# Kernel tuning notes

Hardware: AMD Instinct MI355X
Metric: run time of the kernel (lower is better)

The kernel has to match this reference:

```python
import jax, jax.numpy as jnp
import numpy as np

EPS = 1e-5  # BatchNorm eps


def _conv(x, w, pad):
    # NCHW / OIHW stride-1 convolution (matches nn.Conv2d(..., padding=pad, bias=False))
    return jax.lax.conv_general_dilated(
        x, w, window_strides=(1, 1), padding=[(pad, pad), (pad, pad)],
        dimension_numbers=("NCHW", "OIHW", "NCHW"))


def _bn2d(x, g, b, m, v):
    # inference-mode BN folded to a per-channel affine
    s = g * jax.lax.rsqrt(v + EPS)
    return x * s[None, :, None, None] + (b - m * s)[None, :, None, None]


def _pool2(x):
    # AvgPool2d(2): non-overlapping 2x2 mean
    n, c, h, w = x.shape
    return x.reshape(n, c, h // 2, 2, w // 2, 2).mean(axis=(3, 5))


def _block(x, w, g, b, m, v):
    # Conv -> BN -> ReLU -> AvgPool2 -> Hardtanh(0,1)
    x = _conv(x, w, pad=2)
    x = _bn2d(x, g, b, m, v)
    x = jax.nn.relu(x)
    x = _pool2(x)
    return jnp.clip(x, 0.0, 1.0)


def setup_inputs() -> dict:
    key = jax.random.key(0)
    ks = jax.random.split(key, 24)
    B = 1024
    x = jax.random.uniform(ks[0], (B, 3, 32, 32), dtype=jnp.float32)

    def wgt(k, shape):
        fan_in = shape[1] * shape[2] * shape[3]
        return jax.random.normal(k, shape, jnp.float32) / np.float32(np.sqrt(fan_in))

    def bn(k, c):
        k1, k2, k3, k4 = jax.random.split(k, 4)
        g = jax.random.uniform(k1, (c,), jnp.float32, 0.5, 1.5)
        b = jax.random.normal(k2, (c,), jnp.float32) * 0.1
        m = jax.random.normal(k3, (c,), jnp.float32) * 0.1
        v = jax.random.uniform(k4, (c,), jnp.float32, 0.5, 1.5)
        return g, b, m, v

    w1 = wgt(ks[1], (32, 3, 5, 5))
    w2 = wgt(ks[2], (32, 32, 5, 5))
    w3 = wgt(ks[3], (64, 32, 5, 5))
    w4 = wgt(ks[4], (10, 64, 4, 4))  # fc1 as a 4x4 valid conv
    g1, b1, m1, v1 = bn(ks[5], 32)
    g2, b2, m2, v2 = bn(ks[6], 32)
    g3, b3, m3, v3 = bn(ks[7], 64)
    g4, b4, m4, v4 = bn(ks[8], 10)
    return dict(x=x,
                w1=w1, g1=g1, b1=b1, m1=m1, v1=v1,
                w2=w2, g2=g2, b2=b2, m2=m2, v2=v2,
                w3=w3, g3=g3, b3=b3, m3=m3, v3=v3,
                w4=w4, g4=g4, b4=b4, m4=m4, v4=v4)


def reference(x,
              w1, g1, b1, m1, v1,
              w2, g2, b2, m2, v2,
              w3, g3, b3, m3, v3,
              w4, g4, b4, m4, v4):
    x = _block(x, w1, g1, b1, m1, v1)   # [B,32,16,16]
    x = _block(x, w2, g2, b2, m2, v2)   # [B,32,8,8]
    x = _block(x, w3, g3, b3, m3, v3)   # [B,64,4,4]
    x = _conv(x, w4, pad=0)             # [B,10,1,1]
    x = x.reshape(x.shape[0], -1)       # flatten -> [B,10]
    s = g4 * jax.lax.rsqrt(v4 + EPS)    # BatchNorm1d_fixed (inference affine)
    return x * s[None, :] + (b4 - m4 * s)[None, :]
```

## Files before the change

### kernel.cpp

```cpp
#include <hip/hip_runtime.h>
#include <hip/hip_bf16.h>

#define EPS 1e-5f

typedef __bf16 v8bf __attribute__((ext_vector_type(8)));
typedef __bf16 v4bf __attribute__((ext_vector_type(4)));
typedef float  v4f  __attribute__((ext_vector_type(4)));

__global__ void k_wtrans(const float* __restrict__ w1, const float* __restrict__ w2,
                         const float* __restrict__ w3,
                         __hip_bfloat16* __restrict__ fb1, __hip_bfloat16* __restrict__ fb2,
                         __hip_bfloat16* __restrict__ fb3)
{
    int idx = blockIdx.x * 256 + threadIdx.x;
    if (idx < 640) {
        int lane = idx & 63, fi = idx >> 6;
        int ky = fi >> 1, nt = fi & 1;
        int oc = nt * 16 + (lane & 15), k0 = (lane >> 4) * 8;
        __hip_bfloat16* dst = fb1 + idx * 8;
        #pragma unroll
        for (int j = 0; j < 8; ++j) {
            int k = k0 + j, dx = k >> 2, ic = k & 3;
            float val = (dx < 5 && ic < 3) ? w1[oc * 75 + ic * 25 + ky * 5 + dx] : 0.f;
            dst[j] = __float2bfloat16(val);
        }
    } else if (idx < 640 + 3200) {
        int k2 = idx - 640;
        int lane = k2 & 63, fi = k2 >> 6;
        int tap = fi >> 1, nt = fi & 1;
        int oc = nt * 16 + (lane & 15), ic0 = (lane >> 4) * 8;
        __hip_bfloat16* dst = fb2 + k2 * 8;
        #pragma unroll
        for (int j = 0; j < 8; ++j)
            dst[j] = __float2bfloat16(w2[oc * 800 + (ic0 + j) * 25 + tap]);
    } else if (idx < 640 + 3200 + 6400) {
        int k3 = idx - 3840;
        int lane = k3 & 63, fi = k3 >> 6;
        int tap = fi >> 2, nt = fi & 3;
        int oc = nt * 16 + (lane & 15), ic0 = (lane >> 4) * 8;
        __hip_bfloat16* dst = fb3 + k3 * 8;
        #pragma unroll
        for (int j = 0; j < 8; ++j)
            dst[j] = __float2bfloat16(w3[oc * 800 + (ic0 + j) * 25 + tap]);
    }
}

__global__ __launch_bounds__(256, 3) void k_fused(
    const float* __restrict__ x,
    const __hip_bfloat16* __restrict__ fb1,
    const __hip_bfloat16* __restrict__ fb2,
    const __hip_bfloat16* __restrict__ fb3,
    const float* __restrict__ w4,
    const float* __restrict__ g1, const float* __restrict__ b1,
    const float* __restrict__ m1, const float* __restrict__ v1,
    const float* __restrict__ g2, const float* __restrict__ b2,
    const float* __restrict__ m2, const float* __restrict__ v2,
    const float* __restrict__ g3, const float* __restrict__ b3,
    const float* __restrict__ m3, const float* __restrict__ v3,
    const float* __restrict__ g4, const float* __restrict__ b4,
    const float* __restrict__ m4, const float* __restrict__ v4,
    float* __restrict__ out)
{
    __shared__ __align__(16) unsigned char pool[43840];
    __shared__ float sc1[32], bi1[32], sc2[32], bi2[32], sc3[64], bi3[64];

    __hip_bfloat16 (*xs2)[20][40] = (__hip_bfloat16(*)[20][40])pool;
    __hip_bfloat16 (*xs1)[40][4]  = (__hip_bfloat16(*)[40][4])(pool + 32000);
    __hip_bfloat16 (*xs3)[12][40] = (__hip_bfloat16(*)[12][40])(pool + 32000);
    float* fin = (float*)pool;

    const int img = blockIdx.x, t = threadIdx.x;
    const int lane = t & 63, wave = t >> 6;
    const int lo = lane & 15, hi = lane >> 4;

    for (int i = t; i < 2740; i += 256) ((uint4*)pool)[i] = make_uint4(0, 0, 0, 0);
    if (t < 32) {
        float s = g1[t] * rsqrtf(v1[t] + EPS); sc1[t] = s; bi1[t] = b1[t] - m1[t] * s;
        float u = g2[t] * rsqrtf(v2[t] + EPS); sc2[t] = u; bi2[t] = b2[t] - m2[t] * u;
    }
    if (t < 64) {
        float s = g3[t] * rsqrtf(v3[t] + EPS); sc3[t] = s; bi3[t] = b3[t] - m3[t] * s;
    }
    __syncthreads();

    #pragma unroll
    for (int it = 0; it < 3; ++it) {
        int i = t + it * 256;
        float4 val = *(const float4*)(x + (size_t)img * 3072 + i * 4);
        int ic = i >> 8, rem = i & 255;
        int y = rem >> 3, xx = (rem & 7) * 4;
        xs1[y + 2][xx + 2][ic] = __float2bfloat16(val.x);
        xs1[y + 2][xx + 3][ic] = __float2bfloat16(val.y);
        xs1[y + 2][xx + 4][ic] = __float2bfloat16(val.z);
        xs1[y + 2][xx + 5][ic] = __float2bfloat16(val.w);
    }
    __syncthreads();

    {
        v8bf bw[5][2];
        #pragma unroll
        for (int ky = 0; ky < 5; ++ky)
            #pragma unroll
            for (int nt = 0; nt < 2; ++nt)
                bw[ky][nt] = *(const v8bf*)(fb1 + ((ky * 2 + nt) * 64 + lane) * 8);

        #pragma unroll
        for (int pi = 0; pi < 4; ++pi) {
            const int pr = wave + pi * 4;
            const int y0 = 2 * pr;
            v4f acc[2][2][2];
            #pragma unroll
            for (int a0 = 0; a0 < 2; ++a0)
                #pragma unroll
                for (int a1 = 0; a1 < 2; ++a1)
                    #pragma unroll
                    for (int a2 = 0; a2 < 2; ++a2)
                        acc[a0][a1][a2] = (v4f){0.f, 0.f, 0.f, 0.f};

            #pragma unroll
            for (int xh = 0; xh < 2; ++xh) {
                const int xx = xh * 16 + lo + hi * 2;
                v8bf av[6];
                #pragma unroll
                for (int r = 0; r < 6; ++r) {
                    v4bf lo4 = *(const v4bf*)&xs1[y0 + r][xx][0];
                    v4bf hi4 = *(const v4bf*)&xs1[y0 + r][xx + 1][0];
                    av[r] = __builtin_shufflevector(lo4, hi4, 0, 1, 2, 3, 4, 5, 6, 7);
                }
                #pragma unroll
                for (int ky = 0; ky < 5; ++ky) {
                    acc[0][xh][0] = __builtin_amdgcn_mfma_f32_16x16x32_bf16(av[ky],     bw[ky][0], acc[0][xh][0], 0, 0, 0);
                    acc[0][xh][1] = __builtin_amdgcn_mfma_f32_16x16x32_bf16(av[ky],     bw[ky][1], acc[0][xh][1], 0, 0, 0);
                    acc[1][xh][0] = __builtin_amdgcn_mfma_f32_16x16x32_bf16(av[ky + 1], bw[ky][0], acc[1][xh][0], 0, 0, 0);
                    acc[1][xh][1] = __builtin_amdgcn_mfma_f32_16x16x32_bf16(av[ky + 1], bw[ky][1], acc[1][xh][1], 0, 0, 0);
                }
            }
            #pragma unroll
            for (int xh = 0; xh < 2; ++xh)
                #pragma unroll
                for (int nt = 0; nt < 2; ++nt) {
                    const int oc = nt * 16 + lo;
                    const float s = sc1[oc], bb = bi1[oc];
                    float u0 = fmaxf(fmaf(acc[0][xh][nt][0], s, bb), 0.f);
                    float u1 = fmaxf(fmaf(acc[0][xh][nt][1], s, bb), 0.f);
                    float u2 = fmaxf(fmaf(acc[0][xh][nt][2], s, bb), 0.f);
                    float u3 = fmaxf(fmaf(acc[0][xh][nt][3], s, bb), 0.f);
                    float q0 = fmaxf(fmaf(acc[1][xh][nt][0], s, bb), 0.f);
                    float q1 = fmaxf(fmaf(acc[1][xh][nt][1], s, bb), 0.f);
                    float q2 = fmaxf(fmaf(acc[1][xh][nt][2], s, bb), 0.f);
                    float q3 = fmaxf(fmaf(acc[1][xh][nt][3], s, bb), 0.f);
                    float p0 = fminf(0.25f * (u0 + u1 + q0 + q1), 1.f);
                    float p1 = fminf(0.25f * (u2 + u3 + q2 + q3), 1.f);
                    const int px = xh * 8 + hi * 2;
                    xs2[pr + 2][px + 2][oc] = __float2bfloat16(p0);
                    xs2[pr + 2][px + 3][oc] = __float2bfloat16(p1);
                }
        }
    }
    __syncthreads();

    {
        uint4* p3 = (uint4*)(pool + 32000);
        for (int i = t; i < 720; i += 256) p3[i] = make_uint4(0, 0, 0, 0);
    }
    __syncthreads();

    {
        const int nt = wave & 1, wgrp = wave >> 1;
        v4f acc[4][2];
        #pragma unroll
        for (int a0 = 0; a0 < 4; ++a0)
            #pragma unroll
            for (int a1 = 0; a1 < 2; ++a1)
                acc[a0][a1] = (v4f){0.f, 0.f, 0.f, 0.f};

        for (int kx = 0; kx < 5; ++kx) {
            v8bf bf[5];
            #pragma unroll
            for (int ky = 0; ky < 5; ++ky)
                bf[ky] = *(const v8bf*)(fb2 + ((ky * 5 + kx) * 2 + nt) * 512 + lane * 8);
            #pragma unroll
            for (int rpi = 0; rpi < 4; ++rpi) {
                const int rbase = (wgrp * 4 + rpi) * 2;
                v8bf av[6];
                #pragma unroll
                for (int r = 0; r < 6; ++r)
                    av[r] = *(const v8bf*)&xs2[rbase + r][lo + kx][hi * 8];
                #pragma unroll
                for (int ky = 0; ky < 5; ++ky) {
                    acc[rpi][0] = __builtin_amdgcn_mfma_f32_16x16x32_bf16(av[ky],     bf[ky], acc[rpi][0], 0, 0, 0);
                    acc[rpi][1] = __builtin_amdgcn_mfma_f32_16x16x32_bf16(av[ky + 1], bf[ky], acc[rpi][1], 0, 0, 0);
                }
            }
        }
        const int oc = nt * 16 + lo;
        const float s = sc2[oc], bb = bi2[oc];
        #pragma unroll
        for (int rpi = 0; rpi < 4; ++rpi) {
            const int rp = wgrp * 4 + rpi;
            float u0 = fmaxf(fmaf(acc[rpi][0][0], s, bb), 0.f);
            float u1 = fmaxf(fmaf(acc[rpi][0][1], s, bb), 0.f);
            float u2 = fmaxf(fmaf(acc[rpi][0][2], s, bb), 0.f);
            float u3 = fmaxf(fmaf(acc[rpi][0][3], s, bb), 0.f);
            float q0 = fmaxf(fmaf(acc[rpi][1][0], s, bb), 0.f);
            float q1 = fmaxf(fmaf(acc[rpi][1][1], s, bb), 0.f);
            float q2 = fmaxf(fmaf(acc[rpi][1][2], s, bb), 0.f);
            float q3 = fmaxf(fmaf(acc[rpi][1][3], s, bb), 0.f);
            float p0 = fminf(0.25f * (u0 + u1 + q0 + q1), 1.f);
            float p1 = fminf(0.25f * (u2 + u3 + q2 + q3), 1.f);
            xs3[rp + 2][hi * 2 + 2][oc] = __float2bfloat16(p0);
            xs3[rp + 2][hi * 2 + 3][oc] = __float2bfloat16(p1);
        }
    }
    __syncthreads();

    {
        const int nt = wave;
        const int oc = nt * 16 + lo;
        const int ya0 = lo >> 3, xa = lo & 7;
        v4f acc[4];
        #pragma unroll
        for (int q = 0; q < 4; ++q) acc[q] = (v4f){0.f, 0.f, 0.f, 0.f};

        #pragma unroll
        for (int tap = 0; tap < 25; ++tap) {
            const int ky = tap / 5, kx = tap % 5;
            v8bf bfr = *(const v8bf*)(fb3 + (tap * 4 + nt) * 512 + lane * 8);
            #pragma unroll
            for (int mt = 0; mt < 4; ++mt) {
                v8bf av = *(const v8bf*)&xs3[2 * mt + ya0 + ky][xa + kx][hi * 8];
                acc[mt] = __builtin_amdgcn_mfma_f32_16x16x32_bf16(av, bfr, acc[mt], 0, 0, 0);
            }
        }
        const float s = sc3[oc], bb = bi3[oc];
        const int xb = (hi & 1) * 2;
        #pragma unroll
        for (int mt = 0; mt < 4; ++mt) {
            float v0 = fmaxf(fmaf(acc[mt][0], s, bb), 0.f);
            float v1 = fmaxf(fmaf(acc[mt][1], s, bb), 0.f);
            float v2 = fmaxf(fmaf(acc[mt][2], s, bb), 0.f);
            float v3 = fmaxf(fmaf(acc[mt][3], s, bb), 0.f);
            float s01 = v0 + v1, s23 = v2 + v3;
            float o01 = __shfl_xor(s01, 32);
            float o23 = __shfl_xor(s23, 32);
            float p0 = fminf(0.25f * (s01 + o01), 1.f);
            float p1 = fminf(0.25f * (s23 + o23), 1.f);
            if (hi < 2) {
                fin[oc * 16 + mt * 4 + xb]     = p0;
                fin[oc * 16 + mt * 4 + xb + 1] = p1;
            }
        }
    }
    __syncthreads();

    {
        for (int oc = wave; oc < 10; oc += 4) {
            const float4* wp = (const float4*)(w4 + oc * 1024);
            const float4* fp = (const float4*)fin;
            float acc0 = 0.f, acc1 = 0.f;
            #pragma unroll
            for (int ch = 0; ch < 4; ++ch) {
                float4 a = fp[ch * 64 + lane];
                float4 w = wp[ch * 64 + lane];
                acc0 = fmaf(a.x, w.x, acc0); acc1 = fmaf(a.y, w.y, acc1);
                acc0 = fmaf(a.z, w.z, acc0); acc1 = fmaf(a.w, w.w, acc1);
            }
            float acc = acc0 + acc1;
            acc += __shfl_xor(acc, 1);
            acc += __shfl_xor(acc, 2);
            acc += __shfl_xor(acc, 4);
            acc += __shfl_xor(acc, 8);
            acc += __shfl_xor(acc, 16);
            acc += __shfl_xor(acc, 32);
            if (lane == 0) {
                float s = g4[oc] * rsqrtf(v4[oc] + EPS);
                out[img * 10 + oc] = acc * s + (b4[oc] - m4[oc] * s);
            }
        }
    }
}

extern "C" void kernel_launch(void* const* d_in, const int* in_sizes, int n_in,
                              void* d_out, int out_size, void* d_ws, size_t ws_size,
                              hipStream_t stream) {
    const float* x  = (const float*)d_in[0];
    const float* w1 = (const float*)d_in[1];
    const float* g1 = (const float*)d_in[2];
    const float* b1 = (const float*)d_in[3];
    const float* m1 = (const float*)d_in[4];
    const float* v1 = (const float*)d_in[5];
    const float* w2 = (const float*)d_in[6];
    const float* g2 = (const float*)d_in[7];
    const float* b2 = (const float*)d_in[8];
    const float* m2 = (const float*)d_in[9];
    const float* v2 = (const float*)d_in[10];
    const float* w3 = (const float*)d_in[11];
    const float* g3 = (const float*)d_in[12];
    const float* b3 = (const float*)d_in[13];
    const float* m3 = (const float*)d_in[14];
    const float* v3 = (const float*)d_in[15];
    const float* w4 = (const float*)d_in[16];
    const float* g4 = (const float*)d_in[17];
    const float* b4 = (const float*)d_in[18];
    const float* m4 = (const float*)d_in[19];
    const float* v4 = (const float*)d_in[20];
    float* out = (float*)d_out;

    char* base = (char*)d_ws;
    __hip_bfloat16* fb1 = (__hip_bfloat16*)base;
    __hip_bfloat16* fb2 = (__hip_bfloat16*)(base + 16384);
    __hip_bfloat16* fb3 = (__hip_bfloat16*)(base + 67584);

    k_wtrans<<<40, 256, 0, stream>>>(w1, w2, w3, fb1, fb2, fb3);
    k_fused<<<1024, 256, 0, stream>>>(x, fb1, fb2, fb3, w4,
                                      g1, b1, m1, v1, g2, b2, m2, v2,
                                      g3, b3, m3, v3, g4, b4, m4, v4, out);
}
```

Before: 38.99 us.

## Double workgroup size to 512 threads and split conv work across eight waves

Launches 512 threads per image instead of 256 and gives each of the eight waves half the output tiles in every conv stage. Conv1 waves now hold one output-channel tile, and conv3 waves take half the M tiles. Conv2 and conv3 also prefetch the next kx/ky set of weight fragments into registers while the MFMAs run, and the conv1 weights are loaded before the LDS zeroing. The aim is more waves in flight per image to hide latency, with fewer registers per wave. The cost is more per-block synchronisation and possibly fewer resident blocks per CU, since LDS use stays the same.

```diff
diff --git a/kernel.cpp b/kernel.cpp
--- a/kernel.cpp
+++ b/kernel.cpp
@@ -45,7 +45,7 @@
     }
 }
 
-__global__ __launch_bounds__(256, 3) void k_fused(
+__global__ __launch_bounds__(512, 4) void k_fused(
     const float* __restrict__ x,
     const __hip_bfloat16* __restrict__ fb1,
     const __hip_bfloat16* __restrict__ fb2,
@@ -73,7 +73,13 @@
     const int lane = t & 63, wave = t >> 6;
     const int lo = lane & 15, hi = lane >> 4;
 
-    for (int i = t; i < 2740; i += 256) ((uint4*)pool)[i] = make_uint4(0, 0, 0, 0);
+    const int nt1 = wave & 1;
+    v8bf bw[5];
+    #pragma unroll
+    for (int ky = 0; ky < 5; ++ky)
+        bw[ky] = *(const v8bf*)(fb1 + ((ky * 2 + nt1) * 64 + lane) * 8);
+
+    for (int i = t; i < 2740; i += 512) ((uint4*)pool)[i] = make_uint4(0, 0, 0, 0);
     if (t < 32) {
         float s = g1[t] * rsqrtf(v1[t] + EPS); sc1[t] = s; bi1[t] = b1[t] - m1[t] * s;
         float u = g2[t] * rsqrtf(v2[t] + EPS); sc2[t] = u; bi2[t] = b2[t] - m2[t] * u;
@@ -83,9 +89,7 @@
     }
     __syncthreads();
 
-    #pragma unroll
-    for (int it = 0; it < 3; ++it) {
-        int i = t + it * 256;
+    for (int i = t; i < 768; i += 512) {
         float4 val = *(const float4*)(x + (size_t)img * 3072 + i * 4);
         int ic = i >> 8, rem = i & 255;
         int y = rem >> 3, xx = (rem & 7) * 4;
@@ -97,25 +101,17 @@
     __syncthreads();
 
     {
-        v8bf bw[5][2];
-        #pragma unroll
-        for (int ky = 0; ky < 5; ++ky)
-            #pragma unroll
-            for (int nt = 0; nt < 2; ++nt)
-                bw[ky][nt] = *(const v8bf*)(fb1 + ((ky * 2 + nt) * 64 + lane) * 8);
-
+        const int prg = wave >> 1;
         #pragma unroll
         for (int pi = 0; pi < 4; ++pi) {
-            const int pr = wave + pi * 4;
+            const int pr = prg + pi * 4;
             const int y0 = 2 * pr;
-            v4f acc[2][2][2];
+            v4f acc[2][2];
             #pragma unroll
             for (int a0 = 0; a0 < 2; ++a0)
                 #pragma unroll
                 for (int a1 = 0; a1 < 2; ++a1)
-                    #pragma unroll
-                    for (int a2 = 0; a2 < 2; ++a2)
-                        acc[a0][a1][a2] = (v4f){0.f, 0.f, 0.f, 0.f};
+                    acc[a0][a1] = (v4f){0.f, 0.f, 0.f, 0.f};
 
             #pragma unroll
             for (int xh = 0; xh < 2; ++xh) {
@@ -129,75 +125,82 @@
                 }
                 #pragma unroll
                 for (int ky = 0; ky < 5; ++ky) {
-                    acc[0][xh][0] = __builtin_amdgcn_mfma_f32_16x16x32_bf16(av[ky],     bw[ky][0], acc[0][xh][0], 0, 0, 0);
-                    acc[0][xh][1] = __builtin_amdgcn_mfma_f32_16x16x32_bf16(av[ky],     bw[ky][1], acc[0][xh][1], 0, 0, 0);
-                    acc[1][xh][0] = __builtin_amdgcn_mfma_f32_16x16x32_bf16(av[ky + 1], bw[ky][0], acc[1][xh][0], 0, 0, 0);
-                    acc[1][xh][1] = __builtin_amdgcn_mfma_f32_16x16x32_bf16(av[ky + 1], bw[ky][1], acc[1][xh][1], 0, 0, 0);
+                    acc[0][xh] = __builtin_amdgcn_mfma_f32_16x16x32_bf16(av[ky],     bw[ky], acc[0][xh], 0, 0, 0);
+                    acc[1][xh] = __builtin_amdgcn_mfma_f32_16x16x32_bf16(av[ky + 1], bw[ky], acc[1][xh], 0, 0, 0);
                 }
             }
-            #pragma unroll
-            for (int xh = 0; xh < 2; ++xh)
-                #pragma unroll
-                for (int nt = 0; nt < 2; ++nt) {
-                    const int oc = nt * 16 + lo;
-                    const float s = sc1[oc], bb = bi1[oc];
-                    float u0 = fmaxf(fmaf(acc[0][xh][nt][0], s, bb), 0.f);
-                    float u1 = fmaxf(fmaf(acc[0][xh][nt][1], s, bb), 0.f);
-                    float u2 = fmaxf(fmaf(acc[0][xh][nt][2], s, bb), 0.f);
-                    float u3 = fmaxf(fmaf(acc[0][xh][nt][3], s, bb), 0.f);
-                    float q0 = fmaxf(fmaf(acc[1][xh][nt][0], s, bb), 0.f);
-                    float q1 = fmaxf(fmaf(acc[1][xh][nt][1], s, bb), 0.f);
-                    float q2 = fmaxf(fmaf(acc[1][xh][nt][2], s, bb), 0.f);
-                    float q3 = fmaxf(fmaf(acc[1][xh][nt][3], s, bb), 0.f);
-                    float p0 = fminf(0.25f * (u0 + u1 + q0 + q1), 1.f);
-                    float p1 = fminf(0.25f * (u2 + u3 + q2 + q3), 1.f);
-                    const int px = xh * 8 + hi * 2;
-                    xs2[pr + 2][px + 2][oc] = __float2bfloat16(p0);
-                    xs2[pr + 2][px + 3][oc] = __float2bfloat16(p1);
-                }
+            const int oc = nt1 * 16 + lo;
+            const float s = sc1[oc], bb = bi1[oc];
+            #pragma unroll
+            for (int xh = 0; xh < 2; ++xh) {
+                float u0 = fmaxf(fmaf(acc[0][xh][0], s, bb), 0.f);
+                float u1 = fmaxf(fmaf(acc[0][xh][1], s, bb), 0.f);
+                float u2 = fmaxf(fmaf(acc[0][xh][2], s, bb), 0.f);
+                float u3 = fmaxf(fmaf(acc[0][xh][3], s, bb), 0.f);
+                float q0 = fmaxf(fmaf(acc[1][xh][0], s, bb), 0.f);
+                float q1 = fmaxf(fmaf(acc[1][xh][1], s, bb), 0.f);
+                float q2 = fmaxf(fmaf(acc[1][xh][2], s, bb), 0.f);
+                float q3 = fmaxf(fmaf(acc[1][xh][3], s, bb), 0.f);
+                float p0 = fminf(0.25f * (u0 + u1 + q0 + q1), 1.f);
+                float p1 = fminf(0.25f * (u2 + u3 + q2 + q3), 1.f);
+                const int px = xh * 8 + hi * 2;
+                xs2[pr + 2][px + 2][oc] = __float2bfloat16(p0);
+                xs2[pr + 2][px + 3][oc] = __float2bfloat16(p1);
+            }
         }
     }
     __syncthreads();
 
     {
         uint4* p3 = (uint4*)(pool + 32000);
-        for (int i = t; i < 720; i += 256) p3[i] = make_uint4(0, 0, 0, 0);
+        for (int i = t; i < 720; i += 512) p3[i] = make_uint4(0, 0, 0, 0);
     }
     __syncthreads();
 
     {
         const int nt = wave & 1, wgrp = wave >> 1;
-        v4f acc[4][2];
-        #pragma unroll
-        for (int a0 = 0; a0 < 4; ++a0)
+        v4f acc[2][2];
+        #pragma unroll
+        for (int a0 = 0; a0 < 2; ++a0)
             #pragma unroll
             for (int a1 = 0; a1 < 2; ++a1)
                 acc[a0][a1] = (v4f){0.f, 0.f, 0.f, 0.f};
 
+        v8bf bf[5];
+        #pragma unroll
+        for (int ky = 0; ky < 5; ++ky)
+            bf[ky] = *(const v8bf*)(fb2 + ((ky * 5 + 0) * 2 + nt) * 512 + lane * 8);
+
+        #pragma unroll
         for (int kx = 0; kx < 5; ++kx) {
-            v8bf bf[5];
-            #pragma unroll
-            for (int ky = 0; ky < 5; ++ky)
-                bf[ky] = *(const v8bf*)(fb2 + ((ky * 5 + kx) * 2 + nt) * 512 + lane * 8);
-            #pragma unroll
-            for (int rpi = 0; rpi < 4; ++rpi) {
-                const int rbase = (wgrp * 4 + rpi) * 2;
-                v8bf av[6];
-                #pragma unroll
-                for (int r = 0; r < 6; ++r)
-                    av[r] = *(const v8bf*)&xs2[rbase + r][lo + kx][hi * 8];
-                #pragma unroll
-                for (int ky = 0; ky < 5; ++ky) {
-                    acc[rpi][0] = __builtin_amdgcn_mfma_f32_16x16x32_bf16(av[ky],     bf[ky], acc[rpi][0], 0, 0, 0);
-                    acc[rpi][1] = __builtin_amdgcn_mfma_f32_16x16x32_bf16(av[ky + 1], bf[ky], acc[rpi][1], 0, 0, 0);
-                }
-            }
-        }
+            v8bf bfn[5];
+            if (kx < 4) {
+                #pragma unroll
+                for (int ky = 0; ky < 5; ++ky)
+                    bfn[ky] = *(const v8bf*)(fb2 + ((ky * 5 + kx + 1) * 2 + nt) * 512 + lane * 8);
+            }
+            v8bf av[8];
+            #pragma unroll
+            for (int r = 0; r < 8; ++r)
+                av[r] = *(const v8bf*)&xs2[wgrp * 4 + r][lo + kx][hi * 8];
+            #pragma unroll
+            for (int ky = 0; ky < 5; ++ky) {
+                acc[0][0] = __builtin_amdgcn_mfma_f32_16x16x32_bf16(av[ky],     bf[ky], acc[0][0], 0, 0, 0);
+                acc[0][1] = __builtin_amdgcn_mfma_f32_16x16x32_bf16(av[ky + 1], bf[ky], acc[0][1], 0, 0, 0);
+                acc[1][0] = __builtin_amdgcn_mfma_f32_16x16x32_bf16(av[ky + 2], bf[ky], acc[1][0], 0, 0, 0);
+                acc[1][1] = __builtin_amdgcn_mfma_f32_16x16x32_bf16(av[ky + 3], bf[ky], acc[1][1], 0, 0, 0);
+            }
+            if (kx < 4) {
+                #pragma unroll
+                for (int ky = 0; ky < 5; ++ky) bf[ky] = bfn[ky];
+            }
+        }
+
         const int oc = nt * 16 + lo;
         const float s = sc2[oc], bb = bi2[oc];
         #pragma unroll
-        for (int rpi = 0; rpi < 4; ++rpi) {
-            const int rp = wgrp * 4 + rpi;
+        for (int rpi = 0; rpi < 2; ++rpi) {
+            const int rp = wgrp * 2 + rpi;
             float u0 = fmaxf(fmaf(acc[rpi][0][0], s, bb), 0.f);
             float u1 = fmaxf(fmaf(acc[rpi][0][1], s, bb), 0.f);
             float u2 = fmaxf(fmaf(acc[rpi][0][2], s, bb), 0.f);
@@ -215,31 +218,50 @@
     __syncthreads();
 
     {
-        const int nt = wave;
+        const int nt = wave >> 1, mh = wave & 1;
         const int oc = nt * 16 + lo;
         const int ya0 = lo >> 3, xa = lo & 7;
-        v4f acc[4];
-        #pragma unroll
-        for (int q = 0; q < 4; ++q) acc[q] = (v4f){0.f, 0.f, 0.f, 0.f};
-
-        #pragma unroll
-        for (int tap = 0; tap < 25; ++tap) {
-            const int ky = tap / 5, kx = tap % 5;
-            v8bf bfr = *(const v8bf*)(fb3 + (tap * 4 + nt) * 512 + lane * 8);
-            #pragma unroll
-            for (int mt = 0; mt < 4; ++mt) {
-                v8bf av = *(const v8bf*)&xs3[2 * mt + ya0 + ky][xa + kx][hi * 8];
-                acc[mt] = __builtin_amdgcn_mfma_f32_16x16x32_bf16(av, bfr, acc[mt], 0, 0, 0);
-            }
-        }
+        v4f acc[2];
+        #pragma unroll
+        for (int q = 0; q < 2; ++q) acc[q] = (v4f){0.f, 0.f, 0.f, 0.f};
+
+        v8bf bf[5];
+        #pragma unroll
+        for (int kx = 0; kx < 5; ++kx)
+            bf[kx] = *(const v8bf*)(fb3 + ((0 * 5 + kx) * 4 + nt) * 512 + lane * 8);
+
+        #pragma unroll
+        for (int ky = 0; ky < 5; ++ky) {
+            v8bf bfn[5];
+            if (ky < 4) {
+                #pragma unroll
+                for (int kx = 0; kx < 5; ++kx)
+                    bfn[kx] = *(const v8bf*)(fb3 + (((ky + 1) * 5 + kx) * 4 + nt) * 512 + lane * 8);
+            }
+            #pragma unroll
+            for (int kx = 0; kx < 5; ++kx) {
+                #pragma unroll
+                for (int mi = 0; mi < 2; ++mi) {
+                    const int mt = mh * 2 + mi;
+                    v8bf av = *(const v8bf*)&xs3[2 * mt + ya0 + ky][xa + kx][hi * 8];
+                    acc[mi] = __builtin_amdgcn_mfma_f32_16x16x32_bf16(av, bf[kx], acc[mi], 0, 0, 0);
+                }
+            }
+            if (ky < 4) {
+                #pragma unroll
+                for (int kx = 0; kx < 5; ++kx) bf[kx] = bfn[kx];
+            }
+        }
+
         const float s = sc3[oc], bb = bi3[oc];
         const int xb = (hi & 1) * 2;
         #pragma unroll
-        for (int mt = 0; mt < 4; ++mt) {
-            float v0 = fmaxf(fmaf(acc[mt][0], s, bb), 0.f);
-            float v1 = fmaxf(fmaf(acc[mt][1], s, bb), 0.f);
-            float v2 = fmaxf(fmaf(acc[mt][2], s, bb), 0.f);
-            float v3 = fmaxf(fmaf(acc[mt][3], s, bb), 0.f);
+        for (int mi = 0; mi < 2; ++mi) {
+            const int mt = mh * 2 + mi;
+            float v0 = fmaxf(fmaf(acc[mi][0], s, bb), 0.f);
+            float v1 = fmaxf(fmaf(acc[mi][1], s, bb), 0.f);
+            float v2 = fmaxf(fmaf(acc[mi][2], s, bb), 0.f);
+            float v3 = fmaxf(fmaf(acc[mi][3], s, bb), 0.f);
             float s01 = v0 + v1, s23 = v2 + v3;
             float o01 = __shfl_xor(s01, 32);
             float o23 = __shfl_xor(s23, 32);
@@ -254,7 +276,7 @@
     __syncthreads();
 
     {
-        for (int oc = wave; oc < 10; oc += 4) {
+        for (int oc = wave; oc < 10; oc += 8) {
             const float4* wp = (const float4*)(w4 + oc * 1024);
             const float4* fp = (const float4*)fin;
             float acc0 = 0.f, acc1 = 0.f;
@@ -312,7 +334,7 @@
     __hip_bfloat16* fb3 = (__hip_bfloat16*)(base + 67584);
 
     k_wtrans<<<40, 256, 0, stream>>>(w1, w2, w3, fb1, fb2, fb3);
-    k_fused<<<1024, 256, 0, stream>>>(x, fb1, fb2, fb3, w4,
+    k_fused<<<1024, 512, 0, stream>>>(x, fb1, fb2, fb3, w4,
                                       g1, b1, m1, v1, g2, b2, m2, v2,
                                       g3, b3, m3, v3, g4, b4, m4, v4, out);
 }
```

After: 39.93 us. 2.4% more time.

## Use 512-thread blocks and reorganize per-wave tiling across conv stages

Applied to the files above, without the earlier changes.

Doubles the block to 8 waves so the first conv spreads over more waves, each handling two pooled rows with 8 preloaded input rows. Conv2 and conv3 run on only 4 waves. Conv2 now computes both output-channel tiles per wave to reuse the A fragments, and conv3 assigns M tiles per wave with double-buffered B-fragment prefetch. The conv1 weight-fragment load is hoisted ahead of the LDS clear. The intent is more latency hiding and fragment reuse, at the cost of idle waves in the later stages and higher register pressure under launch_bounds(512,4).

```diff
diff --git a/kernel.cpp b/kernel.cpp
--- a/kernel.cpp
+++ b/kernel.cpp
@@ -45,7 +45,7 @@
     }
 }
 
-__global__ __launch_bounds__(256, 3) void k_fused(
+__global__ __launch_bounds__(512, 4) void k_fused(
     const float* __restrict__ x,
     const __hip_bfloat16* __restrict__ fb1,
     const __hip_bfloat16* __restrict__ fb2,
@@ -73,7 +73,14 @@
     const int lane = t & 63, wave = t >> 6;
     const int lo = lane & 15, hi = lane >> 4;
 
-    for (int i = t; i < 2740; i += 256) ((uint4*)pool)[i] = make_uint4(0, 0, 0, 0);
+    v8bf bw[5][2];
+    #pragma unroll
+    for (int ky = 0; ky < 5; ++ky)
+        #pragma unroll
+        for (int nt = 0; nt < 2; ++nt)
+            bw[ky][nt] = *(const v8bf*)(fb1 + ((ky * 2 + nt) * 64 + lane) * 8);
+
+    for (int i = t; i < 2740; i += 512) ((uint4*)pool)[i] = make_uint4(0, 0, 0, 0);
     if (t < 32) {
         float s = g1[t] * rsqrtf(v1[t] + EPS); sc1[t] = s; bi1[t] = b1[t] - m1[t] * s;
         float u = g2[t] * rsqrtf(v2[t] + EPS); sc2[t] = u; bi2[t] = b2[t] - m2[t] * u;
@@ -83,9 +90,7 @@
     }
     __syncthreads();
 
-    #pragma unroll
-    for (int it = 0; it < 3; ++it) {
-        int i = t + it * 256;
+    for (int i = t; i < 768; i += 512) {
         float4 val = *(const float4*)(x + (size_t)img * 3072 + i * 4);
         int ic = i >> 8, rem = i & 255;
         int y = rem >> 3, xx = (rem & 7) * 4;
@@ -97,17 +102,17 @@
     __syncthreads();
 
     {
-        v8bf bw[5][2];
-        #pragma unroll
-        for (int ky = 0; ky < 5; ++ky)
-            #pragma unroll
-            for (int nt = 0; nt < 2; ++nt)
-                bw[ky][nt] = *(const v8bf*)(fb1 + ((ky * 2 + nt) * 64 + lane) * 8);
-
-        #pragma unroll
-        for (int pi = 0; pi < 4; ++pi) {
-            const int pr = wave + pi * 4;
-            const int y0 = 2 * pr;
+        const int y0 = 4 * wave;
+        #pragma unroll
+        for (int xh = 0; xh < 2; ++xh) {
+            const int xx = xh * 16 + lo + hi * 2;
+            v8bf av[8];
+            #pragma unroll
+            for (int r = 0; r < 8; ++r) {
+                v4bf lo4 = *(const v4bf*)&xs1[y0 + r][xx][0];
+                v4bf hi4 = *(const v4bf*)&xs1[y0 + r][xx + 1][0];
+                av[r] = __builtin_shufflevector(lo4, hi4, 0, 1, 2, 3, 4, 5, 6, 7);
+            }
             v4f acc[2][2][2];
             #pragma unroll
             for (int a0 = 0; a0 < 2; ++a0)
@@ -116,41 +121,32 @@
                     #pragma unroll
                     for (int a2 = 0; a2 < 2; ++a2)
                         acc[a0][a1][a2] = (v4f){0.f, 0.f, 0.f, 0.f};
-
-            #pragma unroll
-            for (int xh = 0; xh < 2; ++xh) {
-                const int xx = xh * 16 + lo + hi * 2;
-                v8bf av[6];
-                #pragma unroll
-                for (int r = 0; r < 6; ++r) {
-                    v4bf lo4 = *(const v4bf*)&xs1[y0 + r][xx][0];
-                    v4bf hi4 = *(const v4bf*)&xs1[y0 + r][xx + 1][0];
-                    av[r] = __builtin_shufflevector(lo4, hi4, 0, 1, 2, 3, 4, 5, 6, 7);
+            #pragma unroll
+            for (int ky = 0; ky < 5; ++ky)
+                #pragma unroll
+                for (int nt = 0; nt < 2; ++nt) {
+                    acc[0][0][nt] = __builtin_amdgcn_mfma_f32_16x16x32_bf16(av[ky],     bw[ky][nt], acc[0][0][nt], 0, 0, 0);
+                    acc[0][1][nt] = __builtin_amdgcn_mfma_f32_16x16x32_bf16(av[ky + 1], bw[ky][nt], acc[0][1][nt], 0, 0, 0);
+                    acc[1][0][nt] = __builtin_amdgcn_mfma_f32_16x16x32_bf16(av[ky + 2], bw[ky][nt], acc[1][0][nt], 0, 0, 0);
+                    acc[1][1][nt] = __builtin_amdgcn_mfma_f32_16x16x32_bf16(av[ky + 3], bw[ky][nt], acc[1][1][nt], 0, 0, 0);
                 }
-                #pragma unroll
-                for (int ky = 0; ky < 5; ++ky) {
-                    acc[0][xh][0] = __builtin_amdgcn_mfma_f32_16x16x32_bf16(av[ky],     bw[ky][0], acc[0][xh][0], 0, 0, 0);
-                    acc[0][xh][1] = __builtin_amdgcn_mfma_f32_16x16x32_bf16(av[ky],     bw[ky][1], acc[0][xh][1], 0, 0, 0);
-                    acc[1][xh][0] = __builtin_amdgcn_mfma_f32_16x16x32_bf16(av[ky + 1], bw[ky][0], acc[1][xh][0], 0, 0, 0);
-                    acc[1][xh][1] = __builtin_amdgcn_mfma_f32_16x16x32_bf16(av[ky + 1], bw[ky][1], acc[1][xh][1], 0, 0, 0);
-                }
-            }
-            #pragma unroll
-            for (int xh = 0; xh < 2; ++xh)
+            #pragma unroll
+            for (int pri = 0; pri < 2; ++pri)
                 #pragma unroll
                 for (int nt = 0; nt < 2; ++nt) {
                     const int oc = nt * 16 + lo;
                     const float s = sc1[oc], bb = bi1[oc];
-                    float u0 = fmaxf(fmaf(acc[0][xh][nt][0], s, bb), 0.f);
-                    float u1 = fmaxf(fmaf(acc[0][xh][nt][1], s, bb), 0.f);
-                    float u2 = fmaxf(fmaf(acc[0][xh][nt][2], s, bb), 0.f);
-                    float u3 = fmaxf(fmaf(acc[0][xh][nt][3], s, bb), 0.f);
-                    float q0 = fmaxf(fmaf(acc[1][xh][nt][0], s, bb), 0.f);
-                    float q1 = fmaxf(fmaf(acc[1][xh][nt][1], s, bb), 0.f);
-                    float q2 = fmaxf(fmaf(acc[1][xh][nt][2], s, bb), 0.f);
-                    float q3 = fmaxf(fmaf(acc[1][xh][nt][3], s, bb), 0.f);
+                    float u0 = fmaxf(fmaf(acc[pri][0][nt][0], s, bb), 0.f);
+                    float u1 = fmaxf(fmaf(acc[pri][0][nt][1], s, bb), 0.f);
+                    float u2 = fmaxf(fmaf(acc[pri][0][nt][2], s, bb), 0.f);
+                    float u3 = fmaxf(fmaf(acc[pri][0][nt][3], s, bb), 0.f);
+                    float q0 = fmaxf(fmaf(acc[pri][1][nt][0], s, bb), 0.f);
+                    float q1 = fmaxf(fmaf(acc[pri][1][nt][1], s, bb), 0.f);
+                    float q2 = fmaxf(fmaf(acc[pri][1][nt][2], s, bb), 0.f);
+                    float q3 = fmaxf(fmaf(acc[pri][1][nt][3], s, bb), 0.f);
                     float p0 = fminf(0.25f * (u0 + u1 + q0 + q1), 1.f);
                     float p1 = fminf(0.25f * (u2 + u3 + q2 + q3), 1.f);
+                    const int pr = 2 * wave + pri;
                     const int px = xh * 8 + hi * 2;
                     xs2[pr + 2][px + 2][oc] = __float2bfloat16(p0);
                     xs2[pr + 2][px + 3][oc] = __float2bfloat16(p1);
@@ -161,85 +157,102 @@
 
     {
         uint4* p3 = (uint4*)(pool + 32000);
-        for (int i = t; i < 720; i += 256) p3[i] = make_uint4(0, 0, 0, 0);
-    }
-    __syncthreads();
-
-    {
-        const int nt = wave & 1, wgrp = wave >> 1;
-        v4f acc[4][2];
-        #pragma unroll
-        for (int a0 = 0; a0 < 4; ++a0)
+        for (int i = t; i < 720; i += 512) p3[i] = make_uint4(0, 0, 0, 0);
+    }
+    __syncthreads();
+
+    if (wave < 4) {
+        v4f acc[2][2][2];
+        #pragma unroll
+        for (int a0 = 0; a0 < 2; ++a0)
             #pragma unroll
             for (int a1 = 0; a1 < 2; ++a1)
-                acc[a0][a1] = (v4f){0.f, 0.f, 0.f, 0.f};
-
+                #pragma unroll
+                for (int a2 = 0; a2 < 2; ++a2)
+                    acc[a0][a1][a2] = (v4f){0.f, 0.f, 0.f, 0.f};
+
+        #pragma unroll
         for (int kx = 0; kx < 5; ++kx) {
-            v8bf bf[5];
+            v8bf bf[5][2];
             #pragma unroll
             for (int ky = 0; ky < 5; ++ky)
-                bf[ky] = *(const v8bf*)(fb2 + ((ky * 5 + kx) * 2 + nt) * 512 + lane * 8);
-            #pragma unroll
-            for (int rpi = 0; rpi < 4; ++rpi) {
-                const int rbase = (wgrp * 4 + rpi) * 2;
-                v8bf av[6];
-                #pragma unroll
-                for (int r = 0; r < 6; ++r)
-                    av[r] = *(const v8bf*)&xs2[rbase + r][lo + kx][hi * 8];
-                #pragma unroll
-                for (int ky = 0; ky < 5; ++ky) {
-                    acc[rpi][0] = __builtin_amdgcn_mfma_f32_16x16x32_bf16(av[ky],     bf[ky], acc[rpi][0], 0, 0, 0);
-                    acc[rpi][1] = __builtin_amdgcn_mfma_f32_16x16x32_bf16(av[ky + 1], bf[ky], acc[rpi][1], 0, 0, 0);
+                #pragma unroll
+                for (int nt = 0; nt < 2; ++nt)
+                    bf[ky][nt] = *(const v8bf*)(fb2 + ((ky * 5 + kx) * 2 + nt) * 512 + lane * 8);
+            v8bf av[8];
+            #pragma unroll
+            for (int r = 0; r < 8; ++r)
+                av[r] = *(const v8bf*)&xs2[4 * wave + r][lo + kx][hi * 8];
+            #pragma unroll
+            for (int ky = 0; ky < 5; ++ky)
+                #pragma unroll
+                for (int nt = 0; nt < 2; ++nt) {
+                    acc[0][0][nt] = __builtin_amdgcn_mfma_f32_16x16x32_bf16(av[ky],     bf[ky][nt], acc[0][0][nt], 0, 0, 0);
+                    acc[0][1][nt] = __builtin_amdgcn_mfma_f32_16x16x32_bf16(av[ky + 1], bf[ky][nt], acc[0][1][nt], 0, 0, 0);
+                    acc[1][0][nt] = __builtin_amdgcn_mfma_f32_16x16x32_bf16(av[ky + 2], bf[ky][nt], acc[1][0][nt], 0, 0, 0);
+                    acc[1][1][nt] = __builtin_amdgcn_mfma_f32_16x16x32_bf16(av[ky + 3], bf[ky][nt], acc[1][1][nt], 0, 0, 0);
                 }
-            }
-        }
-        const int oc = nt * 16 + lo;
-        const float s = sc2[oc], bb = bi2[oc];
-        #pragma unroll
-        for (int rpi = 0; rpi < 4; ++rpi) {
-            const int rp = wgrp * 4 + rpi;
-            float u0 = fmaxf(fmaf(acc[rpi][0][0], s, bb), 0.f);
-            float u1 = fmaxf(fmaf(acc[rpi][0][1], s, bb), 0.f);
-            float u2 = fmaxf(fmaf(acc[rpi][0][2], s, bb), 0.f);
-            float u3 = fmaxf(fmaf(acc[rpi][0][3], s, bb), 0.f);
-            float q0 = fmaxf(fmaf(acc[rpi][1][0], s, bb), 0.f);
-            float q1 = fmaxf(fmaf(acc[rpi][1][1], s, bb), 0.f);
-            float q2 = fmaxf(fmaf(acc[rpi][1][2], s, bb), 0.f);
-            float q3 = fmaxf(fmaf(acc[rpi][1][3], s, bb), 0.f);
-            float p0 = fminf(0.25f * (u0 + u1 + q0 + q1), 1.f);
-            float p1 = fminf(0.25f * (u2 + u3 + q2 + q3), 1.f);
-            xs3[rp + 2][hi * 2 + 2][oc] = __float2bfloat16(p0);
-            xs3[rp + 2][hi * 2 + 3][oc] = __float2bfloat16(p1);
-        }
-    }
-    __syncthreads();
-
-    {
-        const int nt = wave;
-        const int oc = nt * 16 + lo;
+        }
+
+        #pragma unroll
+        for (int pri = 0; pri < 2; ++pri)
+            #pragma unroll
+            for (int nt = 0; nt < 2; ++nt) {
+                const int oc = nt * 16 + lo;
+                const float s = sc2[oc], bb = bi2[oc];
+                float u0 = fmaxf(fmaf(acc[pri][0][nt][0], s, bb), 0.f);
+                float u1 = fmaxf(fmaf(acc[pri][0][nt][1], s, bb), 0.f);
+                float u2 = fmaxf(fmaf(acc[pri][0][nt][2], s, bb), 0.f);
+                float u3 = fmaxf(fmaf(acc[pri][0][nt][3], s, bb), 0.f);
+                float q0 = fmaxf(fmaf(acc[pri][1][nt][0], s, bb), 0.f);
+                float q1 = fmaxf(fmaf(acc[pri][1][nt][1], s, bb), 0.f);
+                float q2 = fmaxf(fmaf(acc[pri][1][nt][2], s, bb), 0.f);
+                float q3 = fmaxf(fmaf(acc[pri][1][nt][3], s, bb), 0.f);
+                float p0 = fminf(0.25f * (u0 + u1 + q0 + q1), 1.f);
+                float p1 = fminf(0.25f * (u2 + u3 + q2 + q3), 1.f);
+                const int rp = 2 * wave + pri;
+                xs3[rp + 2][hi * 2 + 2][oc] = __float2bfloat16(p0);
+                xs3[rp + 2][hi * 2 + 3][oc] = __float2bfloat16(p1);
+            }
+    }
+    __syncthreads();
+
+    if (wave < 4) {
+        const int mt = wave;
         const int ya0 = lo >> 3, xa = lo & 7;
         v4f acc[4];
         #pragma unroll
         for (int q = 0; q < 4; ++q) acc[q] = (v4f){0.f, 0.f, 0.f, 0.f};
 
+        v8bf bb[2][4];
+        #pragma unroll
+        for (int nt = 0; nt < 4; ++nt)
+            bb[0][nt] = *(const v8bf*)(fb3 + nt * 512 + lane * 8);
+
         #pragma unroll
         for (int tap = 0; tap < 25; ++tap) {
+            const int cur = tap & 1;
+            if (tap < 24) {
+                #pragma unroll
+                for (int nt = 0; nt < 4; ++nt)
+                    bb[cur ^ 1][nt] = *(const v8bf*)(fb3 + ((tap + 1) * 4 + nt) * 512 + lane * 8);
+            }
             const int ky = tap / 5, kx = tap % 5;
-            v8bf bfr = *(const v8bf*)(fb3 + (tap * 4 + nt) * 512 + lane * 8);
-            #pragma unroll
-            for (int mt = 0; mt < 4; ++mt) {
-                v8bf av = *(const v8bf*)&xs3[2 * mt + ya0 + ky][xa + kx][hi * 8];
-                acc[mt] = __builtin_amdgcn_mfma_f32_16x16x32_bf16(av, bfr, acc[mt], 0, 0, 0);
-            }
-        }
-        const float s = sc3[oc], bb = bi3[oc];
+            v8bf av = *(const v8bf*)&xs3[2 * mt + ya0 + ky][xa + kx][hi * 8];
+            #pragma unroll
+            for (int nt = 0; nt < 4; ++nt)
+                acc[nt] = __builtin_amdgcn_mfma_f32_16x16x32_bf16(av, bb[cur][nt], acc[nt], 0, 0, 0);
+        }
+
         const int xb = (hi & 1) * 2;
         #pragma unroll
-        for (int mt = 0; mt < 4; ++mt) {
-            float v0 = fmaxf(fmaf(acc[mt][0], s, bb), 0.f);
-            float v1 = fmaxf(fmaf(acc[mt][1], s, bb), 0.f);
-            float v2 = fmaxf(fmaf(acc[mt][2], s, bb), 0.f);
-            float v3 = fmaxf(fmaf(acc[mt][3], s, bb), 0.f);
+        for (int nt = 0; nt < 4; ++nt) {
+            const int oc = nt * 16 + lo;
+            const float s = sc3[oc], bb2_ = bi3[oc];
+            float v0 = fmaxf(fmaf(acc[nt][0], s, bb2_), 0.f);
+            float v1 = fmaxf(fmaf(acc[nt][1], s, bb2_), 0.f);
+            float v2 = fmaxf(fmaf(acc[nt][2], s, bb2_), 0.f);
+            float v3 = fmaxf(fmaf(acc[nt][3], s, bb2_), 0.f);
             float s01 = v0 + v1, s23 = v2 + v3;
             float o01 = __shfl_xor(s01, 32);
             float o23 = __shfl_xor(s23, 32);
@@ -254,7 +267,7 @@
     __syncthreads();
 
     {
-        for (int oc = wave; oc < 10; oc += 4) {
+        for (int oc = wave; oc < 10; oc += 8) {
             const float4* wp = (const float4*)(w4 + oc * 1024);
             const float4* fp = (const float4*)fin;
             float acc0 = 0.f, acc1 = 0.f;
@@ -312,7 +325,7 @@
     __hip_bfloat16* fb3 = (__hip_bfloat16*)(base + 67584);
 
     k_wtrans<<<40, 256, 0, stream>>>(w1, w2, w3, fb1, fb2, fb3);
-    k_fused<<<1024, 256, 0, stream>>>(x, fb1, fb2, fb3, w4,
+    k_fused<<<1024, 512, 0, stream>>>(x, fb1, fb2, fb3, w4,
                                       g1, b1, m1, v1, g2, b2, m2, v2,
                                       g3, b3, m3, v3, g4, b4, m4, v4, out);
 }
```

New measurement: 49.94 us. 1.28x slower.
